# Performance work log

Measured on AMD Instinct MI355X. Metric: run time of the kernel, lower is better.

Reference implementation:

```python
import jax, jax.numpy as jnp
import numpy as np

B, T, E, L, V = 16, 1024, 768, 2, 50257
LN_EPS = 1e-5


def setup_inputs() -> dict:
    key = jax.random.key(0)
    ks = jax.random.split(key, 5)
    idx = jax.random.randint(ks[0], (B, T), 0, V)
    wte = jax.random.normal(ks[1], (V, E), dtype=jnp.float32) * 0.02
    Wih = jax.random.normal(ks[2], (L, 3 * E, E), dtype=jnp.float32) * 0.02
    Whh = jax.random.normal(ks[3], (L, 3 * E, E), dtype=jnp.float32) * 0.02
    bih = jnp.zeros((L, 3 * E), dtype=jnp.float32)
    bhh = jnp.zeros((L, 3 * E), dtype=jnp.float32)
    g = jnp.ones((E,), dtype=jnp.float32)
    return {"idx": idx, "wte": wte, "Wih": Wih, "bih": bih,
            "Whh": Whh, "bhh": bhh, "g": g}


def _gru_forward(idx, wte, Wih, bih, Whh, bhh, g):
    x = wte[idx]                       # [B,T,E] token embeddings (dropout=0 -> identity)

    def step(h, xt):                   # h: [L,B,E], xt: [B,E]
        inp = xt
        new_h = []
        for l in range(L):             # small fixed layer loop
            gi = inp @ Wih[l].T + bih[l]       # [B,3E]
            gh = h[l] @ Whh[l].T + bhh[l]      # [B,3E]
            i_r, i_z, i_n = jnp.split(gi, 3, axis=-1)
            h_r, h_z, h_n = jnp.split(gh, 3, axis=-1)
            r = jax.nn.sigmoid(i_r + h_r)
            z = jax.nn.sigmoid(i_z + h_z)
            n = jnp.tanh(i_n + r * h_n)
            hl = (1.0 - z) * n + z * h[l]
            new_h.append(hl)
            inp = hl
        return jnp.stack(new_h), inp   # carry, top-layer output at this t

    h0 = jnp.zeros((L, B, E), dtype=x.dtype)
    _, outs = jax.lax.scan(step, h0, jnp.swapaxes(x, 0, 1))  # outs: [T,B,E]

    # targets=None path: LayerNorm (no bias) + lm_head on the LAST position only
    last = outs[-1]                    # [B,E]
    mu = jnp.mean(last, axis=-1, keepdims=True)
    var = jnp.mean(jnp.square(last - mu), axis=-1, keepdims=True)
    ln = (last - mu) * jax.lax.rsqrt(var + LN_EPS) * g
    logits = ln @ wte.T                # tied lm_head, [B,V]
    return logits[:, None, :]          # [B,1,V]


def reference(idx, wte, Wih, bih, Whh, bhh, g):
    return _gru_forward(idx, wte, Wih, bih, Whh, bhh, g)
```

## Files before the change

### kernel.cpp

```cpp
#include <hip/hip_runtime.h>
#include <hip/hip_fp16.h>
#include <math.h>

#define Bz 16
#define Tz 1024
#define Ez 768
#define E3 2304
#define Vz 50257
#define NBK 256
#define LN_EPS 1e-5f
#define VEC (Bz*Ez)
#define VECW 6144
#define EP 772
#define BS 8
#define CW 12

__device__ __forceinline__ float dot4acc(float acc, float4 w, float4 h){
  acc = fmaf(w.x,h.x,acc); acc = fmaf(w.y,h.y,acc);
  acc = fmaf(w.z,h.z,acc); acc = fmaf(w.w,h.w,acc);
  return acc;
}
__device__ __forceinline__ float sigm(float x){ return 1.0f/(1.0f+expf(-x)); }

__device__ __forceinline__ unsigned pack2(float a, float b){
  __half2 h = __floats2half2_rn(a, b);
  union{__half2 h2; unsigned u;} cv; cv.h2 = h; return cv.u;
}
__device__ __forceinline__ float2 unpack2(unsigned u){
  union{unsigned u; __half2 h2;} cv; cv.u = u;
  return __half22float2(cv.h2);
}


__device__ __forceinline__ void stage8(const unsigned* __restrict__ src,
                                       float (*dst)[EP], int tid){
#pragma unroll
  for (int k=0;k<2;k++){
    const int u0 = tid + k*1536;
    const int u1 = u0 + 512;
    const int u2 = u0 + 1024;
    const unsigned a0 = __hip_atomic_load(src+u0, __ATOMIC_RELAXED, __HIP_MEMORY_SCOPE_AGENT);
    const unsigned a1 = __hip_atomic_load(src+u1, __ATOMIC_RELAXED, __HIP_MEMORY_SCOPE_AGENT);
    const unsigned a2 = __hip_atomic_load(src+u2, __ATOMIC_RELAXED, __HIP_MEMORY_SCOPE_AGENT);
    {const int b=u0/384, c=(u0-b*384)<<1; const float2 f=unpack2(a0); dst[b][c]=f.x; dst[b][c+1]=f.y;}
    {const int b=u1/384, c=(u1-b*384)<<1; const float2 f=unpack2(a1); dst[b][c]=f.x; dst[b][c+1]=f.y;}
    {const int b=u2/384, c=(u2-b*384)<<1; const float2 f=unpack2(a2); dst[b][c]=f.x; dst[b][c+1]=f.y;}
  }
}

__device__ __forceinline__ void stage8x2(const unsigned* __restrict__ srcX,
                                         float (*dstX)[EP],
                                         const unsigned* __restrict__ srcH,
                                         float (*dstH)[EP], int tid){
#pragma unroll
  for (int k=0;k<3;k++){
    const int u0 = tid + (k<<10);
    const int u1 = u0 + 512;
    const unsigned x0 = __hip_atomic_load(srcX+u0, __ATOMIC_RELAXED, __HIP_MEMORY_SCOPE_AGENT);
    const unsigned x1 = __hip_atomic_load(srcX+u1, __ATOMIC_RELAXED, __HIP_MEMORY_SCOPE_AGENT);
    const unsigned h0 = __hip_atomic_load(srcH+u0, __ATOMIC_RELAXED, __HIP_MEMORY_SCOPE_AGENT);
    const unsigned h1 = __hip_atomic_load(srcH+u1, __ATOMIC_RELAXED, __HIP_MEMORY_SCOPE_AGENT);
    const int b0=u0/384, c0_=(u0-b0*384)<<1;
    const int b1=u1/384, c1_=(u1-b1*384)<<1;
    {const float2 f=unpack2(x0); dstX[b0][c0_]=f.x; dstX[b0][c0_+1]=f.y;}
    {const float2 f=unpack2(x1); dstX[b1][c1_]=f.x; dstX[b1][c1_+1]=f.y;}
    {const float2 f=unpack2(h0); dstH[b0][c0_]=f.x; dstH[b0][c0_+1]=f.y;}
    {const float2 f=unpack2(h1); dstH[b1][c1_]=f.x; dstH[b1][c1_+1]=f.y;}
  }
}

__device__ __forceinline__ void zero8(float (*dst)[EP], int tid){
#pragma unroll
  for (int k=0;k<6;k++){
    const int u = tid + (k<<9);
    const int b = u/384, c = (u-b*384)<<1;
    dst[b][c] = 0.f; dst[b][c+1] = 0.f;
  }
}

__device__ __forceinline__ void mm9(const float (*V)[EP],
                                    const float* const (&wRow)[9],
                                    float (*gOut)[9],
                                    int wv4, int kq, int bb){
  float acc[9][2];
#pragma unroll
  for (int r=0;r<9;r++){ acc[r][0]=0.f; acc[r][1]=0.f; }
#pragma unroll 4
  for (int j=0;j<12;j++){
    const int kk = (j<<6) + (kq<<2);
    float4 w4[9];
#pragma unroll
    for (int r=0;r<9;r++) w4[r] = *(const float4*)(wRow[r] + kk);
#pragma unroll
    for (int bi=0;bi<2;bi++){
      const float4 hv = *(const float4*)&V[bb*2+bi][kk];
#pragma unroll
      for (int r=0;r<9;r++) acc[r][bi] = dot4acc(acc[r][bi], w4[r], hv);
    }
  }
#pragma unroll
  for (int r=0;r<9;r++)
#pragma unroll
    for (int bi=0;bi<2;bi++){
      float a = acc[r][bi];
      a += __shfl_xor(a,1); a += __shfl_xor(a,2);
      a += __shfl_xor(a,4); a += __shfl_xor(a,8);
      acc[r][bi]=a;
    }
  if (kq==0){
#pragma unroll
    for (int r=0;r<9;r++)
#pragma unroll
      for (int bi=0;bi<2;bi++) gOut[wv4*9+r][bb*2+bi] = acc[r][bi];
  }
}

__global__ __launch_bounds__(512) void gru_scan(
    const int* __restrict__ idx, const float* __restrict__ wte,
    const float* __restrict__ Wih, const float* __restrict__ bih,
    const float* __restrict__ Whh, const float* __restrict__ bhh,
    unsigned* __restrict__ h0g, unsigned* __restrict__ h1g,
    float* __restrict__ h1f,
    unsigned* __restrict__ flags, unsigned* __restrict__ go)
{
  __shared__ float bufX[BS][EP];
  __shared__ float bufH[BS][EP];
  __shared__ float gatesG[36][9];
  __shared__ float gatesI[2][36][9];
  __shared__ float biasS[72];
  __shared__ float hprev[BS][CW];

  const int tid = threadIdx.x, bx = blockIdx.x;
  const int L = bx>>7, sub = bx&127;
  const int bg = sub>>6, cg = sub&63;
  const int c0 = cg*CW, b0 = bg*BS;
  const int wv = tid>>6, lane = tid&63, kq = lane&15, bb = lane>>4;
  const int wv4 = wv & 3;

  const float* WihL = Wih + (size_t)L*E3*Ez;
  const float* WhhL = Whh + (size_t)L*E3*Ez;

  const float* wRow[9];
  {
    const float* Wb = (wv < 4) ? WhhL : WihL;
#pragma unroll
    for (int r=0;r<9;r++){
      const int m = wv4*9 + r, g = m/12, cc = m - g*12;
      wRow[r] = Wb + (size_t)(g*Ez + c0 + cc)*Ez;
    }
  }
  if (tid<72){
    const int mat = tid/36, mm = tid%36, g = mm/12, cc = mm-g*12;
    biasS[tid] = (mat ? bhh : bih)[L*E3 + g*Ez + c0 + cc];
  }
  if (tid<96) hprev[tid&7][tid>>3] = 0.f;

  if (L==0){
#pragma unroll
    for (int k=0;k<3;k++){
      const int i4 = tid + (k<<9);
      const int b = i4/192, c4 = i4 - b*192;
      const int row = idx[(b0+b)*Tz];
      *(float4*)&bufX[b][c4<<2] = *(const float4*)(wte + (size_t)row*Ez + (c4<<2));
    }
    __syncthreads();
    if (wv>=4) mm9(bufX, wRow, gatesI[1], wv4, kq, bb);
    __syncthreads();
#pragma unroll
    for (int k=0;k<3;k++){
      const int i4 = tid + (k<<9);
      const int b = i4/192, c4 = i4 - b*192;
      const int row = idx[(b0+b)*Tz + 1];
      *(float4*)&bufX[b][c4<<2] = *(const float4*)(wte + (size_t)row*Ez + (c4<<2));
    }
  }
  __syncthreads();

  for (int s=0; s<=Tz+1; ++s){
    if (s>0){
      const unsigned tgt = (unsigned)s;
      if (bx==0){
        if (tid<64){
          const unsigned* f = flags + (tid<<2);
          for(;;){
            const unsigned a0 = __hip_atomic_load(f+0, __ATOMIC_RELAXED, __HIP_MEMORY_SCOPE_AGENT);
            const unsigned a1 = __hip_atomic_load(f+1, __ATOMIC_RELAXED, __HIP_MEMORY_SCOPE_AGENT);
            const unsigned a2 = __hip_atomic_load(f+2, __ATOMIC_RELAXED, __HIP_MEMORY_SCOPE_AGENT);
            const unsigned a3 = __hip_atomic_load(f+3, __ATOMIC_RELAXED, __HIP_MEMORY_SCOPE_AGENT);
            const int ok = (a0>=tgt) & (a1>=tgt) & (a2>=tgt) & (a3>=tgt);
            if (__all(ok)) break;
            __builtin_amdgcn_s_sleep(1);
          }
          __hip_atomic_store(go + (tid<<5), tgt,
                             __ATOMIC_RELAXED, __HIP_MEMORY_SCOPE_AGENT);
        }
      } else {
        if (tid==0){
          const unsigned* gp = go + ((bx&63)<<5);
          while (__hip_atomic_load(gp, __ATOMIC_RELAXED, __HIP_MEMORY_SCOPE_AGENT) < tgt)
            __builtin_amdgcn_s_sleep(2);
        }
      }
      __syncthreads();
    }

    const bool gG = (L==0) ? (s<=Tz-1) : (s>=2);
    const bool gI = (L==0) ? (s<=Tz-2) : (s>=1 && s<=Tz);

    if (L==0){
      if (s==0)            zero8(bufH, tid);
      else if (s<=Tz-1)    stage8(h0g + (size_t)((s-1)%3)*VECW + bg*3072, bufH, tid);
    } else {
      const unsigned* x_src = h0g + (size_t)((s-1)%3)*VECW + bg*3072;
      const unsigned* h_src = h1g + (size_t)((s-1)&1)*VECW + bg*3072;
      if (s>=3 && s<=Tz)      stage8x2(x_src, bufX, h_src, bufH, tid);
      else if (s==2)        { stage8(x_src, bufX, tid); zero8(bufH, tid); }
      else if (s==1)          stage8(x_src, bufX, tid);
      else if (s==Tz+1)       stage8(h_src, bufH, tid);
    }
    __syncthreads();

    if (wv<4){ if (gG) mm9(bufH, wRow, gatesG,        wv4, kq, bb); }
    else     { if (gI) mm9(bufX, wRow, gatesI[s&1],   wv4, kq, bb); }
    __syncthreads();

    if (gG && tid<48){
      const int b = tid&7, j = tid>>3;
      float hv2[2];
#pragma unroll
      for (int e=0;e<2;e++){
        const int cc = 2*j+e;
        const float gir = gatesI[(s-1)&1][cc    ][b] + biasS[cc];
        const float giz = gatesI[(s-1)&1][12+cc][b] + biasS[12+cc];
        const float gin = gatesI[(s-1)&1][24+cc][b] + biasS[24+cc];
        const float ghr = gatesG[cc    ][b] + biasS[36+cc];
        const float ghz = gatesG[12+cc][b] + biasS[48+cc];
        const float ghn = gatesG[24+cc][b] + biasS[60+cc];
        const float r = sigm(gir+ghr);
        const float z = sigm(giz+ghz);
        const float n = tanhf(fmaf(r, ghn, gin));
        const float hp = hprev[b][cc];
        hv2[e] = fmaf(z, hp - n, n);
        hprev[b][cc] = hv2[e];
      }
      const unsigned pk = pack2(hv2[0], hv2[1]);
      if (L==0){
        unsigned* hOutW = h0g + (size_t)(s%3)*VECW;
        __hip_atomic_store(hOutW + (b0+b)*384 + cg*6 + j, pk,
                           __ATOMIC_RELAXED, __HIP_MEMORY_SCOPE_AGENT);
      } else {
        unsigned* hOutW = h1g + (size_t)((s-2)&1)*VECW;
        __hip_atomic_store(hOutW + (b0+b)*384 + cg*6 + j, pk,
                           __ATOMIC_RELAXED, __HIP_MEMORY_SCOPE_AGENT);
        if (s==Tz+1){
          h1f[(b0+b)*Ez + c0 + 2*j    ] = hv2[0];
          h1f[(b0+b)*Ez + c0 + 2*j + 1] = hv2[1];
        }
      }
    }

    __syncthreads();
    if (tid==0)
      __hip_atomic_store(flags + bx, (unsigned)(s+1),
                         __ATOMIC_RELAXED, __HIP_MEMORY_SCOPE_AGENT);

    if (L==0 && s<=Tz-3){
#pragma unroll
      for (int k=0;k<3;k++){
        const int i4 = tid + (k<<9);
        const int b = i4/192, c4 = i4 - b*192;
        const int row = idx[(b0+b)*Tz + (s+2)];
        *(float4*)&bufX[b][c4<<2] = *(const float4*)(wte + (size_t)row*Ez + (c4<<2));
      }
    }
  }
}

__global__ __launch_bounds__(256) void finalize_ln(
    const float* __restrict__ h1, const float* __restrict__ g,
    float* __restrict__ ln)
{
  const int tid=threadIdx.x, wv=tid>>6, lane=tid&63;
  for (int b=wv; b<Bz; b+=4){
    float sum=0.f;
    for (int c=lane;c<Ez;c+=64) sum += h1[b*Ez+c];
#pragma unroll
    for (int off=32; off; off>>=1) sum += __shfl_xor(sum, off);
    const float mu = sum/(float)Ez;
    float s2=0.f;
    for (int c=lane;c<Ez;c+=64){ const float d=h1[b*Ez+c]-mu; s2=fmaf(d,d,s2); }
#pragma unroll
    for (int off=32; off; off>>=1) s2 += __shfl_xor(s2, off);
    const float inv = rsqrtf(s2/(float)Ez + LN_EPS);
    for (int c=lane;c<Ez;c+=64) ln[b*Ez+c] = (h1[b*Ez+c]-mu)*inv*g[c];
  }
}

__global__ __launch_bounds__(256) void lm_head(
    const float* __restrict__ ln, const float* __restrict__ wte,
    float* __restrict__ out)
{
  __shared__ float sLn[Bz][EP];
  const int tid=threadIdx.x;
  for (int i4=tid; i4<Bz*Ez/4; i4+=256){
    const int b = i4/(Ez/4), c = (i4 - b*(Ez/4))<<2;
    *(float4*)(&sLn[b][c]) = *(const float4*)(ln + b*Ez + c);
  }
  __syncthreads();
  const int wv=tid>>6, lane=tid&63, rr=lane>>4, cl=lane&15;
  const int vbase = blockIdx.x*64 + wv*16 + rr;
  float acc[4][16];
#pragma unroll
  for (int k=0;k<4;k++)
#pragma unroll
    for (int b=0;b<16;b++) acc[k][b]=0.f;

  for (int j=0;j<12;j++){
    const int c = (cl<<2) + (j<<6);
    float4 w4[4];
#pragma unroll
    for (int k=0;k<4;k++){
      const int v = vbase + 4*k;
      if (v < Vz) w4[k] = *(const float4*)(wte + (size_t)v*Ez + c);
      else { w4[k].x=w4[k].y=w4[k].z=w4[k].w=0.f; }
    }
#pragma unroll
    for (int b=0;b<16;b++){
      const float4 hv = *(const float4*)(&sLn[b][c]);
#pragma unroll
      for (int k=0;k<4;k++) acc[k][b] = dot4acc(acc[k][b], w4[k], hv);
    }
  }
#pragma unroll
  for (int off=1; off<16; off<<=1)
#pragma unroll
    for (int k=0;k<4;k++)
#pragma unroll
      for (int b=0;b<16;b++) acc[k][b] += __shfl_xor(acc[k][b], off);

  if (cl==0){
#pragma unroll
    for (int k=0;k<4;k++){
      const int v = vbase + 4*k;
      if (v < Vz){
#pragma unroll
        for (int b=0;b<16;b++) out[(size_t)b*Vz + v] = acc[k][b];
      }
    }
  }
}

extern "C" void kernel_launch(void* const* d_in, const int* in_sizes, int n_in,
                              void* d_out, int out_size, void* d_ws, size_t ws_size,
                              hipStream_t stream) {
  const int*   idx = (const int*)  d_in[0];
  const float* wte = (const float*)d_in[1];
  const float* Wih = (const float*)d_in[2];
  const float* bih = (const float*)d_in[3];
  const float* Whh = (const float*)d_in[4];
  const float* bhh = (const float*)d_in[5];
  const float* g   = (const float*)d_in[6];
  float* out = (float*)d_out;

  unsigned* flags = (unsigned*)d_ws;
  unsigned* go    = (unsigned*)d_ws + 512;
  unsigned* h0g   = (unsigned*)d_ws + 4096;
  unsigned* h1g   = h0g + 3*VECW;
  float*    h1f   = (float*)(h1g + 2*VECW);
  float*    ln    = h1f + VEC;

  (void)hipMemsetAsync(d_ws, 0, 16384, stream);

  void* args[] = {(void*)&idx,(void*)&wte,(void*)&Wih,(void*)&bih,
                  (void*)&Whh,(void*)&bhh,(void*)&h0g,(void*)&h1g,
                  (void*)&h1f,(void*)&flags,(void*)&go};
  (void)hipLaunchCooperativeKernel((void*)gru_scan, dim3(NBK), dim3(512), args, 0, stream);

  finalize_ln<<<1, 256, 0, stream>>>(h1f, g, ln);
  lm_head<<<786, 256, 0, stream>>>(ln, wte, out);
}
```

Before: 11.93 ms.

## Prefetch layer-1 input after barrier and deepen layer-0 hidden ring buffer

Layer-1 blocks now stage their input (the layer-0 hidden state) into bufX after signalling the flag, so the load overlaps the wait for the next step's barrier instead of sitting on the critical path. Only the layer-1 recurrent state is loaded right after the barrier. To make room, the layer-1 pipeline shifts one step later, the scan runs one extra step, and the layer-0 hidden ring grows from 3 to 4 slots, indexed with a mask instead of a modulo. The cost is one more global step of latency and a larger workspace, plus a possible staleness risk if the prefetched data is read before it is complete.

```diff
diff --git a/kernel.cpp b/kernel.cpp
--- a/kernel.cpp
+++ b/kernel.cpp
@@ -45,27 +45,6 @@
     {const int b=u0/384, c=(u0-b*384)<<1; const float2 f=unpack2(a0); dst[b][c]=f.x; dst[b][c+1]=f.y;}
     {const int b=u1/384, c=(u1-b*384)<<1; const float2 f=unpack2(a1); dst[b][c]=f.x; dst[b][c+1]=f.y;}
     {const int b=u2/384, c=(u2-b*384)<<1; const float2 f=unpack2(a2); dst[b][c]=f.x; dst[b][c+1]=f.y;}
-  }
-}
-
-__device__ __forceinline__ void stage8x2(const unsigned* __restrict__ srcX,
-                                         float (*dstX)[EP],
-                                         const unsigned* __restrict__ srcH,
-                                         float (*dstH)[EP], int tid){
-#pragma unroll
-  for (int k=0;k<3;k++){
-    const int u0 = tid + (k<<10);
-    const int u1 = u0 + 512;
-    const unsigned x0 = __hip_atomic_load(srcX+u0, __ATOMIC_RELAXED, __HIP_MEMORY_SCOPE_AGENT);
-    const unsigned x1 = __hip_atomic_load(srcX+u1, __ATOMIC_RELAXED, __HIP_MEMORY_SCOPE_AGENT);
-    const unsigned h0 = __hip_atomic_load(srcH+u0, __ATOMIC_RELAXED, __HIP_MEMORY_SCOPE_AGENT);
-    const unsigned h1 = __hip_atomic_load(srcH+u1, __ATOMIC_RELAXED, __HIP_MEMORY_SCOPE_AGENT);
-    const int b0=u0/384, c0_=(u0-b0*384)<<1;
-    const int b1=u1/384, c1_=(u1-b1*384)<<1;
-    {const float2 f=unpack2(x0); dstX[b0][c0_]=f.x; dstX[b0][c0_+1]=f.y;}
-    {const float2 f=unpack2(x1); dstX[b1][c1_]=f.x; dstX[b1][c1_+1]=f.y;}
-    {const float2 f=unpack2(h0); dstH[b0][c0_]=f.x; dstH[b0][c0_+1]=f.y;}
-    {const float2 f=unpack2(h1); dstH[b1][c1_]=f.x; dstH[b1][c1_+1]=f.y;}
   }
 }
 
@@ -176,7 +155,7 @@
   }
   __syncthreads();
 
-  for (int s=0; s<=Tz+1; ++s){
+  for (int s=0; s<=Tz+2; ++s){
     if (s>0){
       const unsigned tgt = (unsigned)s;
       if (bx==0){
@@ -204,19 +183,15 @@
       __syncthreads();
     }
 
-    const bool gG = (L==0) ? (s<=Tz-1) : (s>=2);
-    const bool gI = (L==0) ? (s<=Tz-2) : (s>=1 && s<=Tz);
+    const bool gG = (L==0) ? (s<=Tz-1) : (s>=3);
+    const bool gI = (L==0) ? (s<=Tz-2) : (s>=2 && s<=Tz+1);
 
     if (L==0){
       if (s==0)            zero8(bufH, tid);
-      else if (s<=Tz-1)    stage8(h0g + (size_t)((s-1)%3)*VECW + bg*3072, bufH, tid);
+      else if (s<=Tz-1)    stage8(h0g + (size_t)((s-1)&3)*VECW + bg*3072, bufH, tid);
     } else {
-      const unsigned* x_src = h0g + (size_t)((s-1)%3)*VECW + bg*3072;
-      const unsigned* h_src = h1g + (size_t)((s-1)&1)*VECW + bg*3072;
-      if (s>=3 && s<=Tz)      stage8x2(x_src, bufX, h_src, bufH, tid);
-      else if (s==2)        { stage8(x_src, bufX, tid); zero8(bufH, tid); }
-      else if (s==1)          stage8(x_src, bufX, tid);
-      else if (s==Tz+1)       stage8(h_src, bufH, tid);
+      if (s==3)                 zero8(bufH, tid);
+      else if (s>=4 && s<=Tz+2) stage8(h1g + (size_t)((s-4)&1)*VECW + bg*3072, bufH, tid);
     }
     __syncthreads();
 
@@ -245,14 +220,14 @@
       }
       const unsigned pk = pack2(hv2[0], hv2[1]);
       if (L==0){
-        unsigned* hOutW = h0g + (size_t)(s%3)*VECW;
+        unsigned* hOutW = h0g + (size_t)(s&3)*VECW;
         __hip_atomic_store(hOutW + (b0+b)*384 + cg*6 + j, pk,
                            __ATOMIC_RELAXED, __HIP_MEMORY_SCOPE_AGENT);
       } else {
-        unsigned* hOutW = h1g + (size_t)((s-2)&1)*VECW;
+        unsigned* hOutW = h1g + (size_t)((s-3)&1)*VECW;
         __hip_atomic_store(hOutW + (b0+b)*384 + cg*6 + j, pk,
                            __ATOMIC_RELAXED, __HIP_MEMORY_SCOPE_AGENT);
-        if (s==Tz+1){
+        if (s==Tz+2){
           h1f[(b0+b)*Ez + c0 + 2*j    ] = hv2[0];
           h1f[(b0+b)*Ez + c0 + 2*j + 1] = hv2[1];
         }
@@ -264,14 +239,19 @@
       __hip_atomic_store(flags + bx, (unsigned)(s+1),
                          __ATOMIC_RELAXED, __HIP_MEMORY_SCOPE_AGENT);
 
-    if (L==0 && s<=Tz-3){
-#pragma unroll
-      for (int k=0;k<3;k++){
-        const int i4 = tid + (k<<9);
-        const int b = i4/192, c4 = i4 - b*192;
-        const int row = idx[(b0+b)*Tz + (s+2)];
-        *(float4*)&bufX[b][c4<<2] = *(const float4*)(wte + (size_t)row*Ez + (c4<<2));
-      }
+    if (L==0){
+      if (s<=Tz-3){
+#pragma unroll
+        for (int k=0;k<3;k++){
+          const int i4 = tid + (k<<9);
+          const int b = i4/192, c4 = i4 - b*192;
+          const int row = idx[(b0+b)*Tz + (s+2)];
+          *(float4*)&bufX[b][c4<<2] = *(const float4*)(wte + (size_t)row*Ez + (c4<<2));
+        }
+      }
+    } else {
+      if (s>=1 && s<=Tz)
+        stage8(h0g + (size_t)((s-1)&3)*VECW + bg*3072, bufX, tid);
     }
   }
 }
@@ -365,7 +345,7 @@
   unsigned* flags = (unsigned*)d_ws;
   unsigned* go    = (unsigned*)d_ws + 512;
   unsigned* h0g   = (unsigned*)d_ws + 4096;
-  unsigned* h1g   = h0g + 3*VECW;
+  unsigned* h1g   = h0g + 4*VECW;
   float*    h1f   = (float*)(h1g + 2*VECW);
   float*    ln    = h1f + VEC;
 
```

Measured after the change: 10.70 ms. 10.3% less time.
